# Optimization experiments

Measured on AMD Instinct MI355X. Metric: run time of the kernel, lower is better.

The kernel has to match this reference:

```python
import jax, jax.numpy as jnp
import numpy as np

K = 1024   # codebook size
C = 8      # codebook channels
D = K // C # per-channel code dim = 128
BETA = 0.25
B = 8192   # batch of latent vectors, each of size C*D = K


def setup_inputs() -> dict:
    key = jax.random.key(0)
    k1, k2, k3 = jax.random.split(key, 3)
    latents = jax.random.normal(k1, (B, C * D), dtype=jnp.float32)
    # nn.Embedding(K, D) init: uniform(-1/K, 1/K)
    embedding = jax.random.uniform(k2, (K, D), dtype=jnp.float32,
                                   minval=-1.0 / K, maxval=1.0 / K)
    k = jax.random.randint(k3, (C,), 0, 8, dtype=jnp.int32)
    return {"latents": latents, "embedding": embedding, "k": k}


def reference(latents, embedding, k):
    sg = jax.lax.stop_gradient
    flat = latents.reshape(-1, D)                                  # [B*C, D]
    # squared euclidean distance to every code: [B*C, K]
    dist = (jnp.sum(flat ** 2, axis=1, keepdims=True)
            + jnp.sum(embedding ** 2, axis=1)
            - 2.0 * (flat @ embedding.T))
    order = jnp.argsort(dist, axis=1).reshape(-1, C, K)            # [B, C, K]
    # per channel c, pick the k[c]-th nearest code index
    sel = jnp.take_along_axis(order, k[None, :, None], axis=2)[..., 0]  # [B, C]
    # one-hot @ embedding == plain gather of selected rows
    quantized = embedding[sel.reshape(-1)].reshape(latents.shape)  # [B, C*D]
    commitment_loss = jnp.mean((sg(quantized) - latents) ** 2)
    embedding_loss = jnp.mean((quantized - sg(latents)) ** 2)
    vq_loss = BETA * commitment_loss + embedding_loss
    # straight-through estimator
    quantized_st = latents + sg(quantized - latents)
    return quantized_st, vq_loss
```

## Files before the change

### kernel.cpp

```cpp
#include <hip/hip_runtime.h>

#define KDIM   128
#define NELEM  8388608

#define OFF_EBUF 0
#define OFF_ESQ  65536
#define OFF_FSQ  69632
#define OFF_SEL  70144
#define OFF_RED  70656
#define SMEM_SZ  70688

typedef __attribute__((ext_vector_type(8)))  short  short8;
typedef __attribute__((ext_vector_type(8)))  __bf16 bf16x8;
typedef __attribute__((ext_vector_type(4)))  float  f32x4;

__device__ inline ushort f2bf(float f) {
  unsigned u = __builtin_bit_cast(unsigned, f);
  u += 0x7fffu + ((u >> 16) & 1u);
  return (ushort)(u >> 16);
}
__device__ inline f32x4 mfma16(short8 a, short8 b, f32x4 c) {
  return __builtin_amdgcn_mfma_f32_16x16x32_bf16(
      __builtin_bit_cast(bf16x8, a), __builtin_bit_cast(bf16x8, b), c, 0, 0, 0);
}
__device__ inline void gload16(const void* g, void* l) {
  __builtin_amdgcn_global_load_lds(
      (const __attribute__((address_space(1))) unsigned*)g,
      (__attribute__((address_space(3))) unsigned*)l, 16, 0, 0);
}

__global__ void vq_prep(const float* __restrict__ emb, ushort* __restrict__ ebf,
                        float* __restrict__ esqm) {
  int j = blockIdx.x, d = threadIdx.x;
  float v = emb[j * KDIM + d];
  ebf[j * KDIM + (d ^ ((j & 7) << 3))] = f2bf(v);
  float s = v * v;
#pragma unroll
  for (int m = 1; m <= 32; m <<= 1) s += __shfl_xor(s, m);
  __shared__ float w[2];
  if ((threadIdx.x & 63) == 0) w[threadIdx.x >> 6] = s;
  __syncthreads();
  if (threadIdx.x == 0) esqm[j] = -0.5f * (w[0] + w[1]);
}

__global__ __launch_bounds__(256, 2) void vq_main(
    const float* __restrict__ lat, const float* __restrict__ emb,
    const int* __restrict__ ksel, const ushort* __restrict__ ebf,
    const float* __restrict__ esqm, float* __restrict__ out,
    float* __restrict__ partial) {
  __shared__ __align__(16) unsigned char smem[SMEM_SZ];
  float* esqmLds = (float*)(smem + OFF_ESQ);
  float* fsqLds  = (float*)(smem + OFF_FSQ);
  int*   selLds  = (int*)(smem + OFF_SEL);
  float* redL    = (float*)(smem + OFF_RED);
  float* mbuf    = (float*)(smem + OFF_EBUF);

  const int tid = threadIdx.x;
  const int lane = tid & 63, wid = tid >> 6;
  const int gR0 = blockIdx.x * 128;
  const int n = lane & 15, hi = lane >> 4;

  {
    const char* src = (const char*)ebf + tid * 16;
    char* dst = (char*)smem + OFF_EBUF + tid * 16;
#pragma unroll
    for (int q = 0; q < 8; ++q) gload16(src + q * 4096, dst + q * 4096);
  }
  ((float4*)esqmLds)[tid] = ((const float4*)esqm)[tid];

  short8 bfr[2][4];
  float fsqp[2];
#pragma unroll
  for (int ct = 0; ct < 2; ++ct) {
    const float* rp = lat + (size_t)(gR0 + wid * 32 + ct * 16 + n) * KDIM + hi * 8;
    float s = 0.f;
#pragma unroll
    for (int sfr = 0; sfr < 4; ++sfr) {
      float4 v0 = *(const float4*)(rp + sfr * 32);
      float4 v1 = *(const float4*)(rp + sfr * 32 + 4);
      s += v0.x * v0.x + v0.y * v0.y + v0.z * v0.z + v0.w * v0.w
         + v1.x * v1.x + v1.y * v1.y + v1.z * v1.z + v1.w * v1.w;
      short8 b;
      b[0] = (short)f2bf(v0.x); b[1] = (short)f2bf(v0.y);
      b[2] = (short)f2bf(v0.z); b[3] = (short)f2bf(v0.w);
      b[4] = (short)f2bf(v1.x); b[5] = (short)f2bf(v1.y);
      b[6] = (short)f2bf(v1.z); b[7] = (short)f2bf(v1.w);
      bfr[ct][sfr] = b;
    }
    fsqp[ct] = s;
  }
#pragma unroll
  for (int ct = 0; ct < 2; ++ct) {
    float s = fsqp[ct];
    s += __shfl_xor(s, 16);
    s += __shfl_xor(s, 32);
    if (hi == 0) fsqLds[wid * 32 + ct * 16 + n] = s;
  }
  asm volatile("s_waitcnt vmcnt(0)" ::: "memory");
  __syncthreads();

  const int nm = n & 7;
  const int pb = ((hi ^ (nm & 3)) << 4) | (((nm >> 2) & 1) << 6);
  const char* aE0 = (const char*)smem + OFF_EBUF + n * 256 + pb;
  const char* aO0 = (const char*)smem + OFF_EBUF + n * 256 + (pb ^ 64);

  int cidx[4];
#pragma unroll
  for (int r = 0; r < 4; ++r) cidx[r] = hi * 4 + r;

  const float NINF = __builtin_bit_cast(float, 0xFF800000u);
  float top[2][8];
#pragma unroll
  for (int ct = 0; ct < 2; ++ct)
#pragma unroll
    for (int p = 0; p < 8; ++p) top[ct][p] = NINF;
  float kq[2][4];

#pragma unroll 2
  for (int nn = 0; nn < 8; ++nn) {
    const int cb = (nn & 1) * 32768;
    if (nn < 7) {
      const char* src = (const char*)ebf + (nn + 1) * 32768 + tid * 16;
      char* dst = (char*)smem + OFF_EBUF + (((nn + 1) & 1) * 32768) + tid * 16;
#pragma unroll
      for (int q = 0; q < 8; ++q) gload16(src + q * 4096, dst + q * 4096);
    }
    const float* eqb = esqmLds + nn * 128 + hi * 4;
#pragma unroll
    for (int tp = 0; tp < 8; ++tp) {
      f32x4 e = *(const f32x4*)(eqb + tp * 16);
      f32x4 acc0 = e, acc1 = e;
#pragma unroll
      for (int s = 0; s < 4; ++s) {
        const char* ab = ((s & 1) ? aO0 : aE0) + cb + tp * 4096 + (s >> 1) * 128;
        short8 a = *(const short8*)ab;
        acc0 = mfma16(a, bfr[0][s], acc0);
        acc1 = mfma16(a, bfr[1][s], acc1);
      }
      float kn[2][4];
#pragma unroll
      for (int r = 0; r < 4; ++r) {
        kn[0][r] = __builtin_bit_cast(float,
            (__builtin_bit_cast(unsigned, acc0[r]) & 0xFFFFFC00u) | (unsigned)cidx[r]);
        kn[1][r] = __builtin_bit_cast(float,
            (__builtin_bit_cast(unsigned, acc1[r]) & 0xFFFFFC00u) | (unsigned)cidx[r]);
        cidx[r] += 16;
      }
      if ((tp & 1) == 0) {
#pragma unroll
        for (int ct = 0; ct < 2; ++ct)
#pragma unroll
          for (int r = 0; r < 4; ++r) kq[ct][r] = kn[ct][r];
      } else {
#pragma unroll
        for (int ct = 0; ct < 2; ++ct) {
          float x = fmaxf(fmaxf(kq[ct][0], kq[ct][1]), fmaxf(kq[ct][2], kq[ct][3]));
          float y = fmaxf(fmaxf(kn[ct][0], kn[ct][1]), fmaxf(kn[ct][2], kn[ct][3]));
          float key = fmaxf(x, y);
#pragma unroll
          for (int p = 0; p < 8; ++p) {
            float mx = fmaxf(top[ct][p], key);
            key = fminf(top[ct][p], key);
            top[ct][p] = mx;
          }
        }
      }
    }
    if (nn < 7) {
      asm volatile("s_waitcnt vmcnt(0)" ::: "memory");
      __builtin_amdgcn_s_barrier();
    }
  }

  __syncthreads();

#pragma unroll
  for (int ct = 0; ct < 2; ++ct) {
    const int L = wid * 32 + ct * 16 + n;
    const int sl = hi ^ (n & 3);
    float* dst = mbuf + L * 36 + sl * 8;
    *(f32x4*)(dst + 0) = (f32x4){top[ct][0], top[ct][1], top[ct][2], top[ct][3]};
    *(f32x4*)(dst + 4) = (f32x4){top[ct][4], top[ct][5], top[ct][6], top[ct][7]};
  }
  __syncthreads();

  if (tid < 128) {
    const int L = tid, xk = L & 3;
    int kk = ksel[L & 7]; kk = kk < 0 ? 0 : (kk > 7 ? 7 : kk);
    float hh[4]; int ix[4];
#pragma unroll
    for (int j = 0; j < 4; ++j) { hh[j] = mbuf[L * 36 + ((j ^ xk) << 3)]; ix[j] = 0; }
    float sel;
    for (int s = 0;; ++s) {
      sel = fmaxf(fmaxf(hh[0], hh[1]), fmaxf(hh[2], hh[3]));
      if (s == kk) break;
#pragma unroll
      for (int j = 0; j < 4; ++j) {
        if (hh[j] == sel) {
          ++ix[j];
          hh[j] = (ix[j] < 8) ? mbuf[L * 36 + ((j ^ xk) << 3) + ix[j]] : NINF;
        }
      }
    }
    unsigned sb = __builtin_bit_cast(unsigned, sel);
    selLds[L] = (int)(sb & 1023u);
    float val = __builtin_bit_cast(float, sb & 0xFFFFFC00u);
    float rl = fsqLds[L] - 2.0f * val;
#pragma unroll
    for (int m = 1; m <= 32; m <<= 1) rl += __shfl_xor(rl, m);
    if (lane == 0) redL[wid] = rl;
  }
  __syncthreads();
  if (tid == 0) partial[blockIdx.x] = redL[0] + redL[1];

#pragma unroll
  for (int it = 0; it < 16; ++it) {
    int i = tid + it * 256;
    int row = i >> 5, c4 = i & 31;
    int s2 = selLds[row];
    float4 q = *(const float4*)(emb + (size_t)s2 * KDIM + c4 * 4);
    *(float4*)(out + (size_t)(gR0 + row) * KDIM + c4 * 4) = q;
  }
}

__global__ void vq_reduce(const float* __restrict__ p, float* __restrict__ loss) {
  int t = threadIdx.x;
  double s = (double)p[t] + (double)p[t + 256];
#pragma unroll
  for (int m = 1; m <= 32; m <<= 1) s += __shfl_xor(s, m);
  __shared__ double w[4];
  if ((t & 63) == 0) w[t >> 6] = s;
  __syncthreads();
  if (t == 0) loss[0] = (float)((w[0] + w[1] + w[2] + w[3]) * (1.25 / 8388608.0));
}

extern "C" void kernel_launch(void* const* d_in, const int* in_sizes, int n_in,
                              void* d_out, int out_size, void* d_ws, size_t ws_size,
                              hipStream_t stream) {
  const float* lat = (const float*)d_in[0];
  const float* emb = (const float*)d_in[1];
  const int* ksel = (const int*)d_in[2];
  float* out = (float*)d_out;

  ushort* ebf = (ushort*)d_ws;
  float* esqm = (float*)((char*)d_ws + 262144);
  float* partial = (float*)((char*)d_ws + 266240);

  vq_prep<<<1024, 128, 0, stream>>>(emb, ebf, esqm);
  vq_main<<<512, 256, 0, stream>>>(lat, emb, ksel, ebf, esqm, out, partial);
  vq_reduce<<<1, 256, 0, stream>>>(partial, out + NELEM);
}
```

Before: 44.53 us.

## Split codebook scan across four blocks per row tile with global top-8 merge

The main kernel is split into a scan kernel and an output kernel. Each of 2048 scan blocks handles a quarter of the codebook for 128 rows, loads that 64KB slice into LDS once instead of double-buffering eight chunks, and writes a per-quarter sorted top-8 list to global memory. A new output kernel merges the four lists, picks the k-th code, computes the loss partial and gathers the embedding rows. This raises parallelism from 512 to 2048 blocks and drops the in-loop barriers. In exchange it re-reads the latents four times, adds an extra launch, and writes and reads roughly 8MB of intermediate lists.

```diff
diff --git a/kernel.cpp b/kernel.cpp
--- a/kernel.cpp
+++ b/kernel.cpp
@@ -2,13 +2,6 @@
 
 #define KDIM   128
 #define NELEM  8388608
-
-#define OFF_EBUF 0
-#define OFF_ESQ  65536
-#define OFF_FSQ  69632
-#define OFF_SEL  70144
-#define OFF_RED  70656
-#define SMEM_SZ  70688
 
 typedef __attribute__((ext_vector_type(8)))  short  short8;
 typedef __attribute__((ext_vector_type(8)))  __bf16 bf16x8;
@@ -43,33 +36,29 @@
   if (threadIdx.x == 0) esqm[j] = -0.5f * (w[0] + w[1]);
 }
 
-__global__ __launch_bounds__(256, 2) void vq_main(
-    const float* __restrict__ lat, const float* __restrict__ emb,
-    const int* __restrict__ ksel, const ushort* __restrict__ ebf,
-    const float* __restrict__ esqm, float* __restrict__ out,
-    float* __restrict__ partial) {
-  __shared__ __align__(16) unsigned char smem[SMEM_SZ];
-  float* esqmLds = (float*)(smem + OFF_ESQ);
-  float* fsqLds  = (float*)(smem + OFF_FSQ);
-  int*   selLds  = (int*)(smem + OFF_SEL);
-  float* redL    = (float*)(smem + OFF_RED);
-  float* mbuf    = (float*)(smem + OFF_EBUF);
+__global__ __launch_bounds__(256, 2) void vq_scan(
+    const float* __restrict__ lat, const ushort* __restrict__ ebf,
+    const float* __restrict__ esqm, float* __restrict__ fsq_g,
+    float* __restrict__ lists_g) {
+  __shared__ __align__(16) unsigned char smem[66560];
+  float* esqmLds = (float*)(smem + 65536);
+  float* mbuf    = (float*)(smem);
 
   const int tid = threadIdx.x;
   const int lane = tid & 63, wid = tid >> 6;
-  const int gR0 = blockIdx.x * 128;
+  const int q = blockIdx.x & 3, rb = blockIdx.x >> 2;
+  const int gR0 = rb * 128;
   const int n = lane & 15, hi = lane >> 4;
 
   {
-    const char* src = (const char*)ebf + tid * 16;
-    char* dst = (char*)smem + OFF_EBUF + tid * 16;
-#pragma unroll
-    for (int q = 0; q < 8; ++q) gload16(src + q * 4096, dst + q * 4096);
-  }
-  ((float4*)esqmLds)[tid] = ((const float4*)esqm)[tid];
+    const char* src = (const char*)ebf + q * 65536 + tid * 16;
+    char* dst = (char*)smem + tid * 16;
+#pragma unroll
+    for (int p = 0; p < 16; ++p) gload16(src + p * 4096, dst + p * 4096);
+  }
+  if (tid < 64) ((float4*)esqmLds)[tid] = ((const float4*)(esqm + q * 256))[tid];
 
   short8 bfr[2][4];
-  float fsqp[2];
 #pragma unroll
   for (int ct = 0; ct < 2; ++ct) {
     const float* rp = lat + (size_t)(gR0 + wid * 32 + ct * 16 + n) * KDIM + hi * 8;
@@ -87,26 +76,20 @@
       b[6] = (short)f2bf(v1.z); b[7] = (short)f2bf(v1.w);
       bfr[ct][sfr] = b;
     }
-    fsqp[ct] = s;
-  }
-#pragma unroll
-  for (int ct = 0; ct < 2; ++ct) {
-    float s = fsqp[ct];
     s += __shfl_xor(s, 16);
     s += __shfl_xor(s, 32);
-    if (hi == 0) fsqLds[wid * 32 + ct * 16 + n] = s;
+    if (q == 0 && hi == 0) fsq_g[gR0 + wid * 32 + ct * 16 + n] = s;
   }
   asm volatile("s_waitcnt vmcnt(0)" ::: "memory");
   __syncthreads();
 
-  const int nm = n & 7;
-  const int pb = ((hi ^ (nm & 3)) << 4) | (((nm >> 2) & 1) << 6);
-  const char* aE0 = (const char*)smem + OFF_EBUF + n * 256 + pb;
-  const char* aO0 = (const char*)smem + OFF_EBUF + n * 256 + (pb ^ 64);
+  const int pb = ((hi ^ (n & 3)) << 4) | (((n >> 2) & 1) << 6);
+  const char* aE = (const char*)smem + n * 256 + pb;
+  const char* aO = (const char*)smem + n * 256 + (pb ^ 64);
 
   int cidx[4];
 #pragma unroll
-  for (int r = 0; r < 4; ++r) cidx[r] = hi * 4 + r;
+  for (int r = 0; r < 4; ++r) cidx[r] = q * 256 + hi * 4 + r;
 
   const float NINF = __builtin_bit_cast(float, 0xFF800000u);
   float top[2][8];
@@ -116,60 +99,45 @@
     for (int p = 0; p < 8; ++p) top[ct][p] = NINF;
   float kq[2][4];
 
-#pragma unroll 2
-  for (int nn = 0; nn < 8; ++nn) {
-    const int cb = (nn & 1) * 32768;
-    if (nn < 7) {
-      const char* src = (const char*)ebf + (nn + 1) * 32768 + tid * 16;
-      char* dst = (char*)smem + OFF_EBUF + (((nn + 1) & 1) * 32768) + tid * 16;
-#pragma unroll
-      for (int q = 0; q < 8; ++q) gload16(src + q * 4096, dst + q * 4096);
-    }
-    const float* eqb = esqmLds + nn * 128 + hi * 4;
-#pragma unroll
-    for (int tp = 0; tp < 8; ++tp) {
-      f32x4 e = *(const f32x4*)(eqb + tp * 16);
-      f32x4 acc0 = e, acc1 = e;
-#pragma unroll
-      for (int s = 0; s < 4; ++s) {
-        const char* ab = ((s & 1) ? aO0 : aE0) + cb + tp * 4096 + (s >> 1) * 128;
-        short8 a = *(const short8*)ab;
-        acc0 = mfma16(a, bfr[0][s], acc0);
-        acc1 = mfma16(a, bfr[1][s], acc1);
-      }
-      float kn[2][4];
-#pragma unroll
-      for (int r = 0; r < 4; ++r) {
-        kn[0][r] = __builtin_bit_cast(float,
-            (__builtin_bit_cast(unsigned, acc0[r]) & 0xFFFFFC00u) | (unsigned)cidx[r]);
-        kn[1][r] = __builtin_bit_cast(float,
-            (__builtin_bit_cast(unsigned, acc1[r]) & 0xFFFFFC00u) | (unsigned)cidx[r]);
-        cidx[r] += 16;
-      }
-      if ((tp & 1) == 0) {
-#pragma unroll
-        for (int ct = 0; ct < 2; ++ct)
-#pragma unroll
-          for (int r = 0; r < 4; ++r) kq[ct][r] = kn[ct][r];
-      } else {
-#pragma unroll
-        for (int ct = 0; ct < 2; ++ct) {
-          float x = fmaxf(fmaxf(kq[ct][0], kq[ct][1]), fmaxf(kq[ct][2], kq[ct][3]));
-          float y = fmaxf(fmaxf(kn[ct][0], kn[ct][1]), fmaxf(kn[ct][2], kn[ct][3]));
-          float key = fmaxf(x, y);
-#pragma unroll
-          for (int p = 0; p < 8; ++p) {
-            float mx = fmaxf(top[ct][p], key);
-            key = fminf(top[ct][p], key);
-            top[ct][p] = mx;
-          }
+#pragma unroll
+  for (int tp = 0; tp < 16; ++tp) {
+    f32x4 e = *(const f32x4*)(esqmLds + tp * 16 + hi * 4);
+    f32x4 acc0 = e, acc1 = e;
+#pragma unroll
+    for (int s = 0; s < 4; ++s) {
+      const char* ab = ((s & 1) ? aO : aE) + tp * 4096 + (s >> 1) * 128;
+      short8 a = *(const short8*)ab;
+      acc0 = mfma16(a, bfr[0][s], acc0);
+      acc1 = mfma16(a, bfr[1][s], acc1);
+    }
+    float kn[2][4];
+#pragma unroll
+    for (int r = 0; r < 4; ++r) {
+      kn[0][r] = __builtin_bit_cast(float,
+          (__builtin_bit_cast(unsigned, acc0[r]) & 0xFFFFFC00u) | (unsigned)cidx[r]);
+      kn[1][r] = __builtin_bit_cast(float,
+          (__builtin_bit_cast(unsigned, acc1[r]) & 0xFFFFFC00u) | (unsigned)cidx[r]);
+      cidx[r] += 16;
+    }
+    if ((tp & 1) == 0) {
+#pragma unroll
+      for (int ct = 0; ct < 2; ++ct)
+#pragma unroll
+        for (int r = 0; r < 4; ++r) kq[ct][r] = kn[ct][r];
+    } else {
+#pragma unroll
+      for (int ct = 0; ct < 2; ++ct) {
+        float x = fmaxf(fmaxf(kq[ct][0], kq[ct][1]), fmaxf(kq[ct][2], kq[ct][3]));
+        float y = fmaxf(fmaxf(kn[ct][0], kn[ct][1]), fmaxf(kn[ct][2], kn[ct][3]));
+        float key = fmaxf(x, y);
+#pragma unroll
+        for (int p = 0; p < 8; ++p) {
+          float mx = fmaxf(top[ct][p], key);
+          key = fminf(top[ct][p], key);
+          top[ct][p] = mx;
         }
       }
     }
-    if (nn < 7) {
-      asm volatile("s_waitcnt vmcnt(0)" ::: "memory");
-      __builtin_amdgcn_s_barrier();
-    }
   }
 
   __syncthreads();
@@ -177,19 +145,67 @@
 #pragma unroll
   for (int ct = 0; ct < 2; ++ct) {
     const int L = wid * 32 + ct * 16 + n;
-    const int sl = hi ^ (n & 3);
-    float* dst = mbuf + L * 36 + sl * 8;
+    float* dst = mbuf + L * 33 + hi * 8;
     *(f32x4*)(dst + 0) = (f32x4){top[ct][0], top[ct][1], top[ct][2], top[ct][3]};
     *(f32x4*)(dst + 4) = (f32x4){top[ct][4], top[ct][5], top[ct][6], top[ct][7]};
   }
   __syncthreads();
 
   if (tid < 128) {
-    const int L = tid, xk = L & 3;
-    int kk = ksel[L & 7]; kk = kk < 0 ? 0 : (kk > 7 ? 7 : kk);
+    const float* base = mbuf + tid * 33;
     float hh[4]; int ix[4];
 #pragma unroll
-    for (int j = 0; j < 4; ++j) { hh[j] = mbuf[L * 36 + ((j ^ xk) << 3)]; ix[j] = 0; }
+    for (int j = 0; j < 4; ++j) { hh[j] = base[j * 8]; ix[j] = 1; }
+    float o[8];
+#pragma unroll
+    for (int s = 0; s < 8; ++s) {
+      float sel = fmaxf(fmaxf(hh[0], hh[1]), fmaxf(hh[2], hh[3]));
+      o[s] = sel;
+#pragma unroll
+      for (int j = 0; j < 4; ++j) {
+        if (hh[j] == sel) {
+          hh[j] = (ix[j] < 8) ? base[j * 8 + ix[j]] : NINF;
+          ++ix[j];
+        }
+      }
+    }
+    float* dst = lists_g + (size_t)(gR0 + tid) * 32 + q * 8;
+    *(float4*)(dst + 0) = make_float4(o[0], o[1], o[2], o[3]);
+    *(float4*)(dst + 4) = make_float4(o[4], o[5], o[6], o[7]);
+  }
+}
+
+__global__ __launch_bounds__(256) void vq_out(
+    const float* __restrict__ emb, const int* __restrict__ ksel,
+    const float* __restrict__ lists_g, const float* __restrict__ fsq_g,
+    float* __restrict__ out, float* __restrict__ partial) {
+  __shared__ __align__(16) float lbuf[128 * 33];
+  __shared__ int selLds[128];
+  __shared__ float wLds[4];
+
+  const int tid = threadIdx.x;
+  const int lane = tid & 63, wid = tid >> 6;
+  const int rB0 = blockIdx.x * 128;
+  const float NINF = __builtin_bit_cast(float, 0xFF800000u);
+
+#pragma unroll
+  for (int it = 0; it < 4; ++it) {
+    int f4 = tid + it * 256;
+    int f = f4 * 4;
+    int row = f >> 5, col = f & 31;
+    float4 v = *(const float4*)(lists_g + (size_t)rB0 * 32 + f);
+    *(float4*)(&lbuf[row * 33 + col]) = v;
+  }
+  __syncthreads();
+
+  float rl = 0.f;
+  if (tid < 128) {
+    const int row = rB0 + tid;
+    int kk = ksel[row & 7]; kk = kk < 0 ? 0 : (kk > 7 ? 7 : kk);
+    const float* base = lbuf + tid * 33;
+    float hh[4]; int ix[4];
+#pragma unroll
+    for (int j = 0; j < 4; ++j) { hh[j] = base[j * 8]; ix[j] = 1; }
     float sel;
     for (int s = 0;; ++s) {
       sel = fmaxf(fmaxf(hh[0], hh[1]), fmaxf(hh[2], hh[3]));
@@ -197,29 +213,29 @@
 #pragma unroll
       for (int j = 0; j < 4; ++j) {
         if (hh[j] == sel) {
+          hh[j] = (ix[j] < 8) ? base[j * 8 + ix[j]] : NINF;
           ++ix[j];
-          hh[j] = (ix[j] < 8) ? mbuf[L * 36 + ((j ^ xk) << 3) + ix[j]] : NINF;
         }
       }
     }
     unsigned sb = __builtin_bit_cast(unsigned, sel);
-    selLds[L] = (int)(sb & 1023u);
+    selLds[tid] = (int)(sb & 1023u);
     float val = __builtin_bit_cast(float, sb & 0xFFFFFC00u);
-    float rl = fsqLds[L] - 2.0f * val;
-#pragma unroll
-    for (int m = 1; m <= 32; m <<= 1) rl += __shfl_xor(rl, m);
-    if (lane == 0) redL[wid] = rl;
-  }
-  __syncthreads();
-  if (tid == 0) partial[blockIdx.x] = redL[0] + redL[1];
+    rl = fsq_g[row] - 2.0f * val;
+  }
+#pragma unroll
+  for (int m = 1; m <= 32; m <<= 1) rl += __shfl_xor(rl, m);
+  if (lane == 0) wLds[wid] = rl;
+  __syncthreads();
+  if (tid == 0) partial[blockIdx.x] = wLds[0] + wLds[1] + wLds[2] + wLds[3];
 
 #pragma unroll
   for (int it = 0; it < 16; ++it) {
     int i = tid + it * 256;
     int row = i >> 5, c4 = i & 31;
     int s2 = selLds[row];
-    float4 q = *(const float4*)(emb + (size_t)s2 * KDIM + c4 * 4);
-    *(float4*)(out + (size_t)(gR0 + row) * KDIM + c4 * 4) = q;
+    float4 v = *(const float4*)(emb + (size_t)s2 * KDIM + c4 * 4);
+    *(float4*)(out + (size_t)(rB0 + row) * KDIM + c4 * 4) = v;
   }
 }
 
@@ -242,11 +258,14 @@
   const int* ksel = (const int*)d_in[2];
   float* out = (float*)d_out;
 
-  ushort* ebf = (ushort*)d_ws;
-  float* esqm = (float*)((char*)d_ws + 262144);
-  float* partial = (float*)((char*)d_ws + 266240);
+  ushort* ebf     = (ushort*)d_ws;
+  float*  esqm    = (float*)((char*)d_ws + 262144);
+  float*  fsq_g   = (float*)((char*)d_ws + 266240);
+  float*  lists_g = (float*)((char*)d_ws + 528384);
+  float*  partial = (float*)((char*)d_ws + 8916992);
 
   vq_prep<<<1024, 128, 0, stream>>>(emb, ebf, esqm);
-  vq_main<<<512, 256, 0, stream>>>(lat, emb, ksel, ebf, esqm, out, partial);
+  vq_scan<<<2048, 256, 0, stream>>>(lat, ebf, esqm, fsq_g, lists_g);
+  vq_out<<<512, 256, 0, stream>>>(emb, ksel, lists_g, fsq_g, out, partial);
   vq_reduce<<<1, 256, 0, stream>>>(partial, out + NELEM);
 }
```

Result: slower. 61.31 us (+37.7%).
